# Kernel tuning notes

Measured on AMD Instinct MI355X. Metric: run time of the kernel, lower is better.

Reference implementation:

```python
import jax, jax.numpy as jnp
import numpy as np

N, C, EMB_ROWS = 524288, 128, 32
SLOPE = 0.2  # leaky_relu negative slope


def setup_inputs() -> dict:
    key = jax.random.key(0)
    k1, k2, k3, k4, k5 = jax.random.split(key, 5)
    x = jax.random.normal(k1, (N, C), jnp.float32)
    perm = jax.random.permutation(k2, N)  # fixed stand-in for torch.randperm
    depth = jax.random.normal(k3, (EMB_ROWS, 128), jnp.float32)  # Embedding(32,128), N(0,1) init
    fan_in = 2 * C * 2
    bound = 1.0 / np.sqrt(fan_in)
    W = jax.random.uniform(k4, (C, 2 * C, 2), jnp.float32, -bound, bound)  # Conv1d weight (O,I,K)
    b = jax.random.uniform(k5, (C,), jnp.float32, -bound, bound)
    return {"x": x, "depth": depth, "W": W, "b": b, "perm": perm}


def reference(x, depth, W, b, perm):
    c = W.shape[0]
    x = x[perm]                      # random shuffle of rows
    x = x.T.reshape(1, c, -1)        # [1, C, N]
    i = 0
    # Python while over STATIC shapes -> unrolled at trace time (~log2(N) steps)
    while x.shape[-1] > 1:
        L = x.shape[-1]
        e = jnp.broadcast_to(depth[i].reshape(1, 128, 1), (1, 128, L))
        x = jnp.concatenate([x, e], axis=1)   # [1, 2C, L]
        x = jax.lax.conv_general_dilated(
            x, W, window_strides=(1,), padding="VALID",
            dimension_numbers=("NCH", "OIH", "NCH"))  # [1, C, L-1]
        x = x + b.reshape(1, -1, 1)
        x = jnp.where(x >= 0, x, SLOPE * x)   # leaky_relu(0.2)
        if x.shape[-1] == 1:
            break
        # MaxPool1d(2,2): floor(L/2), drops trailing element for odd L
        x = jax.lax.reduce_window(
            x, -jnp.inf, jax.lax.max,
            window_dimensions=(1, 1, 2), window_strides=(1, 1, 2),
            padding="VALID")
        i += 1
    return x.reshape(c, 1).T  # [1, C]
```

## Files before the change

kernel.cpp:

```cpp
#include <hip/hip_runtime.h>
#include <hip/hip_bf16.h>


typedef __bf16 v8bf __attribute__((ext_vector_type(8)));
typedef float v16f __attribute__((ext_vector_type(16)));

#define NBCONV 128
#define NROWS  129
#define NTILES 4

__device__ __forceinline__ ushort f2bf(float f) {
    __hip_bfloat16 h = __float2bfloat16(f);
    return *reinterpret_cast<ushort*>(&h);
}
__device__ __forceinline__ float bf2f(ushort u) {
    __hip_bfloat16 h;
    *reinterpret_cast<ushort*>(&h) = u;
    return __bfloat162float(h);
}
__device__ __forceinline__ unsigned pack2(float lo, float hi) {
    return (unsigned)f2bf(lo) | ((unsigned)f2bf(hi) << 16);
}

__global__ void bias_kernel(const float* __restrict__ W, const float* __restrict__ b,
                            const float* __restrict__ depth, float* __restrict__ Bst) {
    int i = blockIdx.x, o = threadIdx.x;
    const float* Wo = W + (size_t)o * 512 + 256;
    const float* di = depth + (size_t)i * 128;
    float s = b[o];
#pragma unroll 8
    for (int c = 0; c < 128; ++c) s += di[c] * (Wo[2 * c] + Wo[2 * c + 1]);
    Bst[i * 128 + o] = s;
}

__global__ void repack_kernel(const float* __restrict__ W, ushort* __restrict__ A) {
    int o = blockIdx.x, c = threadIdx.x;
    float v = (c < 128) ? W[(size_t)o * 512 + 2 * c] : W[(size_t)o * 512 + 2 * (c - 128) + 1];
    A[o * 256 + c] = f2bf(v);
}

__global__ __launch_bounds__(256)
void stage_mfma(const ushort* __restrict__ Xin,
                const float* __restrict__ x0,
                const int* __restrict__ perm,
                const ushort* __restrict__ A,
                const float* __restrict__ Bst,
                ushort* __restrict__ Y,
                float* __restrict__ out_f,
                int Lin, int Lp, int stage0, int final) {
    __shared__ ushort xs[NROWS * 128];
    __shared__ ushort ps[16 * 128];
    __shared__ int prow[NROWS];

    const int tid = threadIdx.x;
    const int u0 = blockIdx.x * (NBCONV / 2);
    const int t0 = u0 * 2;

    if (stage0) {
        for (int r = tid; r < NROWS; r += 256) {
            int t = t0 + r;
            prow[r] = (t < Lin) ? perm[t] : 0;
        }
        __syncthreads();
    }
    for (int idx = tid; idx < NROWS * 16; idx += 256) {
        int row = idx >> 4, ck = idx & 15;
        int t = t0 + row;
        int dst = row * 128 + ((ck ^ (row & 15)) * 8);
        if (t < Lin) {
            if (stage0) {
                const float* s = x0 + (size_t)prow[row] * 128 + ck * 8;
                float4 a = *(const float4*)s;
                float4 bq = *(const float4*)(s + 4);
                uint4 v;
                v.x = pack2(a.x, a.y);  v.y = pack2(a.z, a.w);
                v.z = pack2(bq.x, bq.y); v.w = pack2(bq.z, bq.w);
                *(uint4*)&xs[dst] = v;
            } else {
                *(uint4*)&xs[dst] = *(const uint4*)&Xin[(size_t)t * 128 + ck * 8];
            }
        } else {
            uint4 z = {0u, 0u, 0u, 0u};
            *(uint4*)&xs[dst] = z;
        }
    }
    __syncthreads();

    const int lane = tid & 63;
    const int w = tid >> 6;
    const int n31 = lane & 31;
    const int h = lane >> 5;

    v8bf af[16];
    {
        const ushort* Arow = A + (size_t)(w * 32 + n31) * 256 + h * 8;
#pragma unroll
        for (int s = 0; s < 16; ++s) af[s] = *(const v8bf*)&Arow[s * 16];
    }
    float bias_r[16];
#pragma unroll
    for (int r = 0; r < 16; ++r) bias_r[r] = Bst[w * 32 + (r & 3) + 8 * (r >> 2) + 4 * h];

    for (int nt = 0; nt < NTILES; ++nt) {
        const int row0 = nt * 32 + n31;
        const ushort* xr0 = &xs[row0 * 128];
        const ushort* xr1 = &xs[(row0 + 1) * 128];
        const int m0 = row0 & 15, m1 = (row0 + 1) & 15;
        v16f acc = {0.f, 0.f, 0.f, 0.f, 0.f, 0.f, 0.f, 0.f,
                    0.f, 0.f, 0.f, 0.f, 0.f, 0.f, 0.f, 0.f};
#pragma unroll
        for (int s = 0; s < 8; ++s) {
            v8bf b0 = *(const v8bf*)&xr0[((2 * s + h) ^ m0) * 8];
            acc = __builtin_amdgcn_mfma_f32_32x32x16_bf16(af[s], b0, acc, 0, 0, 0);
        }
#pragma unroll
        for (int s = 0; s < 8; ++s) {
            v8bf b1 = *(const v8bf*)&xr1[((2 * s + h) ^ m1) * 8];
            acc = __builtin_amdgcn_mfma_f32_32x32x16_bf16(af[8 + s], b1, acc, 0, 0, 0);
        }
        const int ue = n31 >> 1;
        const bool wlane = !(lane & 1);
#pragma unroll
        for (int q = 0; q < 4; ++q) {
            float p[4];
#pragma unroll
            for (int j = 0; j < 4; ++j) {
                int r = 4 * q + j;
                float y = acc[r] + bias_r[r];
                y = (y >= 0.f) ? y : 0.2f * y;
                float y2 = __shfl_xor(y, 1, 64);
                p[j] = fmaxf(y, y2);
            }
            if (wlane) {
                uint2 v;
                v.x = pack2(p[0], p[1]);
                v.y = pack2(p[2], p[3]);
                *(uint2*)&ps[ue * 128 + w * 32 + 8 * q + 4 * h] = v;
            }
        }
        __syncthreads();
        {
            int u_l = tid >> 4, ck = tid & 15;
            int u_g = u0 + nt * 16 + u_l;
            if (u_g < Lp) {
                if (!final) {
                    *(uint4*)&Y[(size_t)u_g * 128 + ck * 8] = *(const uint4*)&ps[u_l * 128 + ck * 8];
                } else if (u_g == 0) {
                    const ushort* p = &ps[ck * 8];
                    float4 o1, o2;
                    o1.x = bf2f(p[0]); o1.y = bf2f(p[1]); o1.z = bf2f(p[2]); o1.w = bf2f(p[3]);
                    o2.x = bf2f(p[4]); o2.y = bf2f(p[5]); o2.z = bf2f(p[6]); o2.w = bf2f(p[7]);
                    *(float4*)&out_f[ck * 8] = o1;
                    *(float4*)&out_f[ck * 8 + 4] = o2;
                }
            }
        }
        __syncthreads();
    }
}

extern "C" void kernel_launch(void* const* d_in, const int* in_sizes, int n_in,
                              void* d_out, int out_size, void* d_ws, size_t ws_size,
                              hipStream_t stream) {
    const float* x     = (const float*)d_in[0];
    const float* depth = (const float*)d_in[1];
    const float* W     = (const float*)d_in[2];
    const float* b     = (const float*)d_in[3];
    const int*   perm  = (const int*)d_in[4];
    float* out = (float*)d_out;

    char* ws = (char*)d_ws;
    float*  Bst = (float*)ws;
    ushort* A   = (ushort*)(ws + 16384);
    ushort* R0  = (ushort*)(ws + 16384 + 65536);
    ushort* R1  = (ushort*)(ws + 16384 + 65536 + (size_t)262143 * 256);

    bias_kernel<<<18, 128, 0, stream>>>(W, b, depth, Bst);
    repack_kernel<<<128, 256, 0, stream>>>(W, A);

    int Lin = 524288;
    const ushort* in = nullptr;
    for (int i = 0; Lin > 1; ++i) {
        int Lp = (Lin - 1) >> 1;
        int final = (Lp == 1) ? 1 : 0;
        ushort* outb = (i & 1) ? R1 : R0;
        int blocks = (Lp + 63) / 64;
        stage_mfma<<<blocks, 256, 0, stream>>>(in, x, perm, A, Bst + i * 128,
                                               outb, out, Lin, Lp, (i == 0) ? 1 : 0, final);
        in = outb;
        Lin = Lp;
    }
}
```

Before: 632.8 us.

## Split stages into specialized kernels and fuse tail stages into one block

Stage 0 gets its own kernel that gathers the permuted rows into LDS and writes the epilogue directly to global memory, with no LDS staging pass and fewer barriers. Middle stages 1–9 drop the LDS tile entirely and read bf16 rows straight from global into the MFMA operands. The final 8 small stages run in a single one-block kernel that ping-pongs between LDS buffers, replacing many tiny launches. The aim is to cut launch overhead and LDS/barrier cost, at the price of uncoalesced direct global loads in the middle stages and running the tail serially on one CU.

Result: slower. 715.7 us (+13.1%).

```diff
diff --git a/kernel.cpp b/kernel.cpp
--- a/kernel.cpp
+++ b/kernel.cpp
@@ -4,23 +4,17 @@
 
 typedef __bf16 v8bf __attribute__((ext_vector_type(8)));
 typedef float v16f __attribute__((ext_vector_type(16)));
-
-#define NBCONV 128
-#define NROWS  129
-#define NTILES 4
 
 __device__ __forceinline__ ushort f2bf(float f) {
     __hip_bfloat16 h = __float2bfloat16(f);
     return *reinterpret_cast<ushort*>(&h);
 }
-__device__ __forceinline__ float bf2f(ushort u) {
-    __hip_bfloat16 h;
-    *reinterpret_cast<ushort*>(&h) = u;
-    return __bfloat162float(h);
-}
 __device__ __forceinline__ unsigned pack2(float lo, float hi) {
     return (unsigned)f2bf(lo) | ((unsigned)f2bf(hi) << 16);
 }
+__device__ __forceinline__ float leaky(float y) { return (y >= 0.f) ? y : 0.2f * y; }
+
+#define ZACC {0.f,0.f,0.f,0.f,0.f,0.f,0.f,0.f,0.f,0.f,0.f,0.f,0.f,0.f,0.f,0.f}
 
 __global__ void bias_kernel(const float* __restrict__ W, const float* __restrict__ b,
                             const float* __restrict__ depth, float* __restrict__ Bst) {
@@ -39,46 +33,72 @@
     A[o * 256 + c] = f2bf(v);
 }
 
+#define WAVE_SETUP()                                                          \
+    const int tid = threadIdx.x;                                              \
+    const int lane = tid & 63;                                                \
+    const int w = tid >> 6;                                                   \
+    const int n31 = lane & 31;                                                \
+    const int h = lane >> 5;                                                  \
+    v8bf af[16];                                                              \
+    {                                                                         \
+        const ushort* Arow = A + (size_t)(w * 32 + n31) * 256 + h * 8;        \
+        _Pragma("unroll")                                                     \
+        for (int s = 0; s < 16; ++s) af[s] = *(const v8bf*)&Arow[s * 16];     \
+    }
+
+#define LOAD_BIAS(Bs)                                                         \
+    float bias_r[16];                                                         \
+    _Pragma("unroll")                                                         \
+    for (int r = 0; r < 16; ++r)                                              \
+        bias_r[r] = (Bs)[w * 32 + (r & 3) + 8 * (r >> 2) + 4 * h];
+
+#define EPILOGUE_STORE_GLOBAL(acc, u, Lp, Y)                                  \
+    {                                                                         \
+        const bool act_ = !(lane & 1) && ((u) < (Lp));                        \
+        _Pragma("unroll")                                                     \
+        for (int q = 0; q < 4; ++q) {                                         \
+            float p_[4];                                                      \
+            _Pragma("unroll")                                                 \
+            for (int j = 0; j < 4; ++j) {                                     \
+                float y = leaky((acc)[4 * q + j] + bias_r[4 * q + j]);        \
+                float y2 = __shfl_xor(y, 1, 64);                              \
+                p_[j] = fmaxf(y, y2);                                         \
+            }                                                                 \
+            if (act_) {                                                       \
+                uint2 v_;                                                     \
+                v_.x = pack2(p_[0], p_[1]);                                   \
+                v_.y = pack2(p_[2], p_[3]);                                   \
+                *(uint2*)&(Y)[(size_t)(u) * 128 + w * 32 + 8 * q + 4 * h] = v_; \
+            }                                                                 \
+        }                                                                     \
+    }
+
 __global__ __launch_bounds__(256)
-void stage_mfma(const ushort* __restrict__ Xin,
-                const float* __restrict__ x0,
-                const int* __restrict__ perm,
-                const ushort* __restrict__ A,
-                const float* __restrict__ Bst,
-                ushort* __restrict__ Y,
-                float* __restrict__ out_f,
-                int Lin, int Lp, int stage0, int final) {
-    __shared__ ushort xs[NROWS * 128];
-    __shared__ ushort ps[16 * 128];
-    __shared__ int prow[NROWS];
-
-    const int tid = threadIdx.x;
-    const int u0 = blockIdx.x * (NBCONV / 2);
+void stage0_kernel(const float* __restrict__ x0, const int* __restrict__ perm,
+                   const ushort* __restrict__ A, const float* __restrict__ Bst,
+                   ushort* __restrict__ Y, int Lin, int Lp) {
+    __shared__ __align__(16) ushort xs[129 * 128];
+    __shared__ int prow[129];
+
+    const int u0 = blockIdx.x * 64;
     const int t0 = u0 * 2;
 
-    if (stage0) {
-        for (int r = tid; r < NROWS; r += 256) {
-            int t = t0 + r;
-            prow[r] = (t < Lin) ? perm[t] : 0;
-        }
-        __syncthreads();
-    }
-    for (int idx = tid; idx < NROWS * 16; idx += 256) {
+    for (int r = threadIdx.x; r < 129; r += 256) {
+        int t = t0 + r;
+        prow[r] = (t < Lin) ? perm[t] : 0;
+    }
+    __syncthreads();
+    for (int idx = threadIdx.x; idx < 129 * 16; idx += 256) {
         int row = idx >> 4, ck = idx & 15;
-        int t = t0 + row;
         int dst = row * 128 + ((ck ^ (row & 15)) * 8);
-        if (t < Lin) {
-            if (stage0) {
-                const float* s = x0 + (size_t)prow[row] * 128 + ck * 8;
-                float4 a = *(const float4*)s;
-                float4 bq = *(const float4*)(s + 4);
-                uint4 v;
-                v.x = pack2(a.x, a.y);  v.y = pack2(a.z, a.w);
-                v.z = pack2(bq.x, bq.y); v.w = pack2(bq.z, bq.w);
-                *(uint4*)&xs[dst] = v;
-            } else {
-                *(uint4*)&xs[dst] = *(const uint4*)&Xin[(size_t)t * 128 + ck * 8];
-            }
+        if (t0 + row < Lin) {
+            const float* s = x0 + (size_t)prow[row] * 128 + ck * 8;
+            float4 a = *(const float4*)s;
+            float4 bq = *(const float4*)(s + 4);
+            uint4 v;
+            v.x = pack2(a.x, a.y);  v.y = pack2(a.z, a.w);
+            v.z = pack2(bq.x, bq.y); v.w = pack2(bq.z, bq.w);
+            *(uint4*)&xs[dst] = v;
         } else {
             uint4 z = {0u, 0u, 0u, 0u};
             *(uint4*)&xs[dst] = z;
@@ -86,76 +106,127 @@
     }
     __syncthreads();
 
-    const int lane = tid & 63;
-    const int w = tid >> 6;
-    const int n31 = lane & 31;
-    const int h = lane >> 5;
-
-    v8bf af[16];
-    {
-        const ushort* Arow = A + (size_t)(w * 32 + n31) * 256 + h * 8;
-#pragma unroll
-        for (int s = 0; s < 16; ++s) af[s] = *(const v8bf*)&Arow[s * 16];
-    }
-    float bias_r[16];
-#pragma unroll
-    for (int r = 0; r < 16; ++r) bias_r[r] = Bst[w * 32 + (r & 3) + 8 * (r >> 2) + 4 * h];
-
-    for (int nt = 0; nt < NTILES; ++nt) {
+    WAVE_SETUP();
+    LOAD_BIAS(Bst);
+
+#pragma unroll
+    for (int nt = 0; nt < 4; ++nt) {
         const int row0 = nt * 32 + n31;
         const ushort* xr0 = &xs[row0 * 128];
         const ushort* xr1 = &xs[(row0 + 1) * 128];
         const int m0 = row0 & 15, m1 = (row0 + 1) & 15;
-        v16f acc = {0.f, 0.f, 0.f, 0.f, 0.f, 0.f, 0.f, 0.f,
-                    0.f, 0.f, 0.f, 0.f, 0.f, 0.f, 0.f, 0.f};
-#pragma unroll
-        for (int s = 0; s < 8; ++s) {
-            v8bf b0 = *(const v8bf*)&xr0[((2 * s + h) ^ m0) * 8];
-            acc = __builtin_amdgcn_mfma_f32_32x32x16_bf16(af[s], b0, acc, 0, 0, 0);
-        }
-#pragma unroll
-        for (int s = 0; s < 8; ++s) {
-            v8bf b1 = *(const v8bf*)&xr1[((2 * s + h) ^ m1) * 8];
-            acc = __builtin_amdgcn_mfma_f32_32x32x16_bf16(af[8 + s], b1, acc, 0, 0, 0);
-        }
-        const int ue = n31 >> 1;
-        const bool wlane = !(lane & 1);
-#pragma unroll
-        for (int q = 0; q < 4; ++q) {
-            float p[4];
-#pragma unroll
-            for (int j = 0; j < 4; ++j) {
-                int r = 4 * q + j;
-                float y = acc[r] + bias_r[r];
-                y = (y >= 0.f) ? y : 0.2f * y;
-                float y2 = __shfl_xor(y, 1, 64);
-                p[j] = fmaxf(y, y2);
+        v16f acc = ZACC;
+#pragma unroll
+        for (int s = 0; s < 8; ++s)
+            acc = __builtin_amdgcn_mfma_f32_32x32x16_bf16(
+                af[s], *(const v8bf*)&xr0[((2 * s + h) ^ m0) * 8], acc, 0, 0, 0);
+#pragma unroll
+        for (int s = 0; s < 8; ++s)
+            acc = __builtin_amdgcn_mfma_f32_32x32x16_bf16(
+                af[8 + s], *(const v8bf*)&xr1[((2 * s + h) ^ m1) * 8], acc, 0, 0, 0);
+        const int u = u0 + nt * 16 + (n31 >> 1);
+        EPILOGUE_STORE_GLOBAL(acc, u, Lp, Y);
+    }
+}
+
+__global__ __launch_bounds__(256)
+void stage_direct(const ushort* __restrict__ Xin, const ushort* __restrict__ A,
+                  const float* __restrict__ Bst, ushort* __restrict__ Y,
+                  int Lin, int Lp) {
+    WAVE_SETUP();
+    LOAD_BIAS(Bst);
+    const int tb = blockIdx.x * 64;
+#pragma unroll
+    for (int nt = 0; nt < 2; ++nt) {
+        const int t = tb + nt * 32 + n31;
+        const int r0 = min(t, Lin - 1), r1 = min(t + 1, Lin - 1);
+        const ushort* p0 = Xin + (size_t)r0 * 128 + h * 8;
+        const ushort* p1 = Xin + (size_t)r1 * 128 + h * 8;
+        v16f acc = ZACC;
+#pragma unroll
+        for (int s = 0; s < 8; ++s)
+            acc = __builtin_amdgcn_mfma_f32_32x32x16_bf16(
+                af[s], *(const v8bf*)&p0[s * 16], acc, 0, 0, 0);
+#pragma unroll
+        for (int s = 0; s < 8; ++s)
+            acc = __builtin_amdgcn_mfma_f32_32x32x16_bf16(
+                af[8 + s], *(const v8bf*)&p1[s * 16], acc, 0, 0, 0);
+        const int u = t >> 1;
+        EPILOGUE_STORE_GLOBAL(acc, u, Lp, Y);
+    }
+}
+
+__global__ __launch_bounds__(256)
+void tail_fused(const ushort* __restrict__ Xg, const ushort* __restrict__ A,
+                const float* __restrict__ BstAll, float* __restrict__ out) {
+    extern __shared__ __align__(16) ushort tbuf[];
+    ushort* buf0 = tbuf;
+    ushort* buf1 = tbuf + 255 * 128;
+
+    WAVE_SETUP();
+
+    int Lin = 511;
+    for (int st = 0; st < 8; ++st) {
+        const int Lp = (Lin - 1) >> 1;
+        LOAD_BIAS(BstAll + (size_t)(10 + st) * 128);
+        ushort* dst = (st & 1) ? buf1 : buf0;
+        const ushort* src = (st & 1) ? buf0 : buf1;
+        const int ntiles = (Lin - 1 + 31) >> 5;
+        for (int ti = 0; ti < ntiles; ++ti) {
+            const int t = ti * 32 + n31;
+            const int r0 = min(t, Lin - 1), r1 = min(t + 1, Lin - 1);
+            v16f acc = ZACC;
+            if (st == 0) {
+                const ushort* p0 = Xg + (size_t)r0 * 128 + h * 8;
+                const ushort* p1 = Xg + (size_t)r1 * 128 + h * 8;
+#pragma unroll
+                for (int s = 0; s < 8; ++s)
+                    acc = __builtin_amdgcn_mfma_f32_32x32x16_bf16(
+                        af[s], *(const v8bf*)&p0[s * 16], acc, 0, 0, 0);
+#pragma unroll
+                for (int s = 0; s < 8; ++s)
+                    acc = __builtin_amdgcn_mfma_f32_32x32x16_bf16(
+                        af[8 + s], *(const v8bf*)&p1[s * 16], acc, 0, 0, 0);
+            } else {
+                const ushort* sr0 = src + r0 * 128;
+                const ushort* sr1 = src + r1 * 128;
+                const int m0 = r0 & 15, m1 = r1 & 15;
+#pragma unroll
+                for (int s = 0; s < 8; ++s)
+                    acc = __builtin_amdgcn_mfma_f32_32x32x16_bf16(
+                        af[s], *(const v8bf*)&sr0[((2 * s + h) ^ m0) * 8], acc, 0, 0, 0);
+#pragma unroll
+                for (int s = 0; s < 8; ++s)
+                    acc = __builtin_amdgcn_mfma_f32_32x32x16_bf16(
+                        af[8 + s], *(const v8bf*)&sr1[((2 * s + h) ^ m1) * 8], acc, 0, 0, 0);
             }
-            if (wlane) {
-                uint2 v;
-                v.x = pack2(p[0], p[1]);
-                v.y = pack2(p[2], p[3]);
-                *(uint2*)&ps[ue * 128 + w * 32 + 8 * q + 4 * h] = v;
-            }
-        }
-        __syncthreads();
-        {
-            int u_l = tid >> 4, ck = tid & 15;
-            int u_g = u0 + nt * 16 + u_l;
-            if (u_g < Lp) {
-                if (!final) {
-                    *(uint4*)&Y[(size_t)u_g * 128 + ck * 8] = *(const uint4*)&ps[u_l * 128 + ck * 8];
-                } else if (u_g == 0) {
-                    const ushort* p = &ps[ck * 8];
-                    float4 o1, o2;
-                    o1.x = bf2f(p[0]); o1.y = bf2f(p[1]); o1.z = bf2f(p[2]); o1.w = bf2f(p[3]);
-                    o2.x = bf2f(p[4]); o2.y = bf2f(p[5]); o2.z = bf2f(p[6]); o2.w = bf2f(p[7]);
-                    *(float4*)&out_f[ck * 8] = o1;
-                    *(float4*)&out_f[ck * 8 + 4] = o2;
+            const int u = t >> 1;
+            const bool act = !(lane & 1) && (u < Lp);
+#pragma unroll
+            for (int q = 0; q < 4; ++q) {
+                float p[4];
+#pragma unroll
+                for (int j = 0; j < 4; ++j) {
+                    float y = leaky(acc[4 * q + j] + bias_r[4 * q + j]);
+                    float y2 = __shfl_xor(y, 1, 64);
+                    p[j] = fmaxf(y, y2);
+                }
+                if (act) {
+                    if (st < 7) {
+                        const int c8 = 4 * w + q;
+                        uint2 v;
+                        v.x = pack2(p[0], p[1]);
+                        v.y = pack2(p[2], p[3]);
+                        *(uint2*)&dst[u * 128 + ((c8 ^ (u & 15)) * 8) + 4 * h] = v;
+                    } else {
+                        float4 o = {p[0], p[1], p[2], p[3]};
+                        *(float4*)&out[w * 32 + 8 * q + 4 * h] = o;
+                    }
                 }
             }
         }
         __syncthreads();
+        Lin = Lp;
     }
 }
 
@@ -178,16 +249,19 @@
     bias_kernel<<<18, 128, 0, stream>>>(W, b, depth, Bst);
     repack_kernel<<<128, 256, 0, stream>>>(W, A);
 
-    int Lin = 524288;
-    const ushort* in = nullptr;
-    for (int i = 0; Lin > 1; ++i) {
+    stage0_kernel<<<4096, 256, 0, stream>>>(x, perm, A, Bst, R0, 524288, 262143);
+
+    int Lin = 262143;
+    const ushort* in = R0;
+    for (int i = 1; i <= 9; ++i) {
         int Lp = (Lin - 1) >> 1;
-        int final = (Lp == 1) ? 1 : 0;
         ushort* outb = (i & 1) ? R1 : R0;
-        int blocks = (Lp + 63) / 64;
-        stage_mfma<<<blocks, 256, 0, stream>>>(in, x, perm, A, Bst + i * 128,
-                                               outb, out, Lin, Lp, (i == 0) ? 1 : 0, final);
+        int blocks = (Lin - 1 + 63) / 64;
+        stage_direct<<<blocks, 256, 0, stream>>>(in, A, Bst + (size_t)i * 128,
+                                                 outb, Lin, Lp);
         in = outb;
         Lin = Lp;
     }
-}
+
+    tail_fused<<<1, 256, (255 + 127) * 128 * 2, stream>>>(in, A, Bst, out);
+}
```
